# Optimization experiments

Hardware: AMD Instinct MI355X
Metric: run time of the kernel (lower is better)

Reference implementation:

```python
import jax, jax.numpy as jnp
import numpy as np
from jax import lax

WIN = 9  # NCC window per axis (default [9]*3)

# 3x3x3 edge/shape kernels, shape [O=1, I=1, 3, 3, 3]
_LAP = np.zeros((3, 3, 3), np.float32)
_LAP[1, 1, 1] = 6.0
_LAP[0, 1, 1] = _LAP[2, 1, 1] = -1.0
_LAP[1, 0, 1] = _LAP[1, 2, 1] = -1.0
_LAP[1, 1, 0] = _LAP[1, 1, 2] = -1.0
LAP_K = jnp.asarray(_LAP)[None, None]

_row = np.array([[-1.0, 0.0, 1.0], [-2.0, 0.0, 2.0], [-1.0, 0.0, 1.0]], np.float32)
SOBEL_X = jnp.asarray(np.stack([_row, _row, _row], axis=0))[None, None]
_plane = np.array([[-1.0, -2.0, -1.0], [-1.0, -2.0, -1.0], [-1.0, -2.0, -1.0]], np.float32)
SOBEL_Y = jnp.asarray(np.stack([_plane, np.zeros((3, 3), np.float32), -_plane], axis=0))[None, None]
_zp = np.array([[-1.0, -1.0, -1.0], [0.0, 0.0, 0.0], [1.0, 1.0, 1.0]], np.float32)
SOBEL_Z = jnp.asarray(np.stack([_zp, 2.0 * _zp, _zp], axis=0))[None, None]


def conv3d(x, k, pad):
    # x: [N,C,D,H,W], k: [O,I,kd,kh,kw]
    return lax.conv_general_dilated(x, k, (1, 1, 1), [(pad, pad)] * 3)


def box_sum(x, win=WIN):
    # Separable all-ones box filter == dense ones conv (same math, fewer FLOPs)
    pad = win // 2
    for axis in range(3):
        kshape = [1, 1, 1, 1, 1]
        kshape[2 + axis] = win
        k = jnp.ones(kshape, x.dtype)
        padding = [(pad, pad) if a == axis else (0, 0) for a in range(3)]
        x = lax.conv_general_dilated(x, k, (1, 1, 1), padding)
    return x


def ncc_vxm(Ii, Ji, win=WIN):
    win_size = float(win ** 3)
    I2, J2, IJ = Ii * Ii, Ji * Ji, Ii * Ji
    I_sum = box_sum(Ii, win)
    J_sum = box_sum(Ji, win)
    I2_sum = box_sum(I2, win)
    J2_sum = box_sum(J2, win)
    IJ_sum = box_sum(IJ, win)
    u_I = I_sum / win_size
    u_J = J_sum / win_size
    cross = IJ_sum - u_J * I_sum - u_I * J_sum + u_I * u_J * win_size
    I_var = I2_sum - 2.0 * u_I * I_sum + u_I * u_I * win_size
    J_var = J2_sum - 2.0 * u_J * J_sum + u_J * u_J * win_size
    cc = cross * cross / (I_var * J_var + 1e-5)
    return -jnp.mean(cc)


def edge_detection(v):
    return conv3d(v, LAP_K, pad=1)


def shape_detection(v):
    gx = conv3d(v, SOBEL_X, pad=1)
    gy = conv3d(v, SOBEL_Y, pad=1)
    gz = conv3d(v, SOBEL_Z, pad=1)
    return jnp.sqrt(gx * gx + gy * gy + gz * gz)


def setup_inputs() -> dict:
    key = jax.random.key(0)
    k1, k2 = jax.random.split(key)
    shape = (1, 1, 160, 192, 160)
    y_true = jax.random.uniform(k1, shape, dtype=jnp.float32)
    y_pred = jax.random.uniform(k2, shape, dtype=jnp.float32)
    return {"y_true": y_true, "y_pred": y_pred}


def reference(y_true, y_pred):
    loss_orig = ncc_vxm(y_true, y_pred)
    loss_edge = ncc_vxm(edge_detection(y_true), edge_detection(y_pred))
    loss_shape = ncc_vxm(shape_detection(y_true), shape_detection(y_pred))
    return 0.8 * loss_orig + 0.1 * loss_edge + 0.1 * loss_shape
```

## Files before the change

### kernel.cpp

```cpp
#include <hip/hip_runtime.h>
#include <hip/hip_fp16.h>
#include <math.h>

#define DD 160
#define HHH 192
#define WWW 160
constexpr int HW = HHH * WWW;
constexpr int NV = DD * HHH * WWW;
constexpr int W4 = WWW / 4;
constexpr int HC = 4;
constexpr int DC = 4;
constexpr int SC = 5;

constexpr int NB_WH  = (W4 * DD * (HHH / HC)) / 256;
constexpr int NB_SO  = (W4 * HHH * (DD / SC)) / 256;
constexpr int NB_LAP = (NV / 4) / 256;
constexpr int NB_DCC = (W4 * HHH * (DD / DC)) / 256;

__device__ __forceinline__ float4 ldg4(const float* __restrict__ p, int idx, bool ok) {
    float4 z = make_float4(0.f, 0.f, 0.f, 0.f);
    return ok ? *(const float4*)(p + idx) : z;
}

__device__ __forceinline__ void st_h4(__half* __restrict__ t, int idx,
                                      float s0, float s1, float s2, float s3) {
    union { __half2 h2[2]; uint2 u; } pk;
    pk.h2[0] = __floats2half2_rn(s0, s1);
    pk.h2[1] = __floats2half2_rn(s2, s3);
    *(uint2*)(t + idx) = pk.u;
}

__device__ __forceinline__ void ld_h4(const __half* __restrict__ t, int idx, float o[4]) {
    union { __half2 h2[2]; uint2 u; } pk;
    pk.u = *(const uint2*)(t + idx);
    o[0] = __low2float(pk.h2[0]); o[1] = __high2float(pk.h2[0]);
    o[2] = __low2float(pk.h2[1]); o[3] = __high2float(pk.h2[1]);
}

__device__ __forceinline__ void lap_body(int t, const float* __restrict__ a,
                                         const float* __restrict__ b,
                                         __half* __restrict__ oa, __half* __restrict__ ob) {
    int w = (t % W4) * 4;
    int h = (t / W4) % HHH;
    int d = t / (W4 * HHH);
    int idx = (d * HHH + h) * WWW + w;
    bool dok0 = d > 0, dok1 = d < DD - 1, hok0 = h > 0, hok1 = h < HHH - 1;
#pragma unroll
    for (int s = 0; s < 2; s++) {
        const float* p = s ? b : a;
        __half* o = s ? ob : oa;
        float4 c = *(const float4*)(p + idx);
        float m1 = (w > 0) ? p[idx - 1] : 0.f;
        float p4 = (w + 4 < WWW) ? p[idx + 4] : 0.f;
        float4 dm = ldg4(p, idx - HW, dok0);
        float4 dp = ldg4(p, idx + HW, dok1);
        float4 hm = ldg4(p, idx - WWW, hok0);
        float4 hp = ldg4(p, idx + WWW, hok1);
        st_h4(o, idx,
              6.f * c.x - (m1 + c.y + dm.x + dp.x + hm.x + hp.x),
              6.f * c.y - (c.x + c.z + dm.y + dp.y + hm.y + hp.y),
              6.f * c.z - (c.y + c.w + dm.z + dp.z + hm.z + hp.z),
              6.f * c.w - (c.z + p4 + dm.w + dp.w + hm.w + hp.w));
    }
}

__device__ __forceinline__ void sobel_slice(const float* __restrict__ p, int s, int h, int w,
                                            float a1[4], float a2[4], float a3[4]) {
#pragma unroll
    for (int k = 0; k < 4; k++) { a1[k] = 0.f; a2[k] = 0.f; a3[k] = 0.f; }
#pragma unroll
    for (int kh = -1; kh <= 1; kh++) {
        int h2 = h + kh;
        if ((unsigned)h2 < (unsigned)HHH) {
            int rb = (s * HHH + h2) * WWW + w;
            float4 cen = *(const float4*)(p + rb);
            float xm = (w > 0) ? p[rb - 1] : 0.f;
            float xp = (w + 4 < WWW) ? p[rb + 4] : 0.f;
            float xv[6] = {xm, cen.x, cen.y, cen.z, cen.w, xp};
            float smh = (kh == 0) ? 2.f : 1.f;
            float grh = (float)kh;
#pragma unroll
            for (int k = 0; k < 4; k++) {
                float gw = xv[k + 2] - xv[k];
                float pw = xv[k] + xv[k + 1] + xv[k + 2];
                float sw = pw + xv[k + 1];
                a1[k] += smh * gw;
                a2[k] += sw;
                a3[k] += grh * pw;
            }
        }
    }
}

__device__ __forceinline__ void sobel_body(int t, const float* __restrict__ a,
                                           const float* __restrict__ b,
                                           __half* __restrict__ oa, __half* __restrict__ ob) {
    int w = (t % W4) * 4;
    int h = (t / W4) % HHH;
    int c = t / (W4 * HHH);
    int d0 = c * SC;

    float A1[2][3][4], A2[2][3][4], A3[2][3][4];
#pragma unroll
    for (int r = 0; r < 2; r++)
#pragma unroll
        for (int j = 0; j < 3; j++)
#pragma unroll
            for (int k = 0; k < 4; k++) { A1[r][j][k] = 0.f; A2[r][j][k] = 0.f; A3[r][j][k] = 0.f; }

#pragma unroll
    for (int i = 0; i < SC + 2; i++) {
        int s = d0 - 1 + i;
#pragma unroll
        for (int r = 0; r < 2; r++)
#pragma unroll
            for (int k = 0; k < 4; k++) {
                A1[r][0][k] = A1[r][1][k]; A2[r][0][k] = A2[r][1][k]; A3[r][0][k] = A3[r][1][k];
                A1[r][1][k] = A1[r][2][k]; A2[r][1][k] = A2[r][2][k]; A3[r][1][k] = A3[r][2][k];
            }
        if (s >= 0 && s < DD) {
            sobel_slice(a, s, h, w, A1[0][2], A2[0][2], A3[0][2]);
            sobel_slice(b, s, h, w, A1[1][2], A2[1][2], A3[1][2]);
        } else {
#pragma unroll
            for (int r = 0; r < 2; r++)
#pragma unroll
                for (int k = 0; k < 4; k++) { A1[r][2][k] = 0.f; A2[r][2][k] = 0.f; A3[r][2][k] = 0.f; }
        }
        if (i >= 2) {
            int d = s - 1;
            int idx = (d * HHH + h) * WWW + w;
            float va[4], vb[4];
#pragma unroll
            for (int k = 0; k < 4; k++) {
                float gx = A1[0][0][k] + A1[0][1][k] + A1[0][2][k];
                float gy = A2[0][2][k] - A2[0][0][k];
                float gz = A3[0][0][k] + 2.f * A3[0][1][k] + A3[0][2][k];
                va[k] = sqrtf(gx * gx + gy * gy + gz * gz);
                gx = A1[1][0][k] + A1[1][1][k] + A1[1][2][k];
                gy = A2[1][2][k] - A2[1][0][k];
                gz = A3[1][0][k] + 2.f * A3[1][1][k] + A3[1][2][k];
                vb[k] = sqrtf(gx * gx + gy * gy + gz * gz);
            }
            st_h4(oa, idx, va[0], va[1], va[2], va[3]);
            st_h4(ob, idx, vb[0], vb[1], vb[2], vb[3]);
        }
    }
}

__device__ __forceinline__ void q5_from(const float x[12], const float y[12], float q[5][4]) {
    float s0 = 0, s1 = 0, s2 = 0, s3 = 0, s4 = 0;
#pragma unroll
    for (int j = 0; j < 9; j++) {
        s0 += x[j]; s1 += y[j];
        s2 += x[j] * x[j]; s3 += y[j] * y[j]; s4 += x[j] * y[j];
    }
    q[0][0] = s0; q[1][0] = s1; q[2][0] = s2; q[3][0] = s3; q[4][0] = s4;
#pragma unroll
    for (int k = 1; k < 4; k++) {
        q[0][k] = q[0][k - 1] + x[k + 8] - x[k - 1];
        q[1][k] = q[1][k - 1] + y[k + 8] - y[k - 1];
        q[2][k] = q[2][k - 1] + x[k + 8] * x[k + 8] - x[k - 1] * x[k - 1];
        q[3][k] = q[3][k - 1] + y[k + 8] * y[k + 8] - y[k - 1] * y[k - 1];
        q[4][k] = q[4][k - 1] + x[k + 8] * y[k + 8] - x[k - 1] * y[k - 1];
    }
}

__device__ __forceinline__ void ld12(const float* __restrict__ p, int rowbase, int w, float x[12]) {
    bool lo = (w >= 4);
    bool hi = (w + 7 < WWW);
    float4 x0 = ldg4(p, rowbase + w - 4, lo);
    float4 x1 = *(const float4*)(p + rowbase + w);
    float4 x2 = ldg4(p, rowbase + w + 4, hi);
    x[0] = x0.x; x[1] = x0.y; x[2] = x0.z; x[3] = x0.w;
    x[4] = x1.x; x[5] = x1.y; x[6] = x1.z; x[7] = x1.w;
    x[8] = x2.x; x[9] = x2.y; x[10] = x2.z; x[11] = x2.w;
}

__device__ __forceinline__ void ld12(const __half* __restrict__ p, int rowbase, int w, float x[12]) {
    bool lo = (w >= 4);
    bool hi = (w + 7 < WWW);
    union { __half2 h2[2]; uint2 u; } u0, u1, u2;
    uint2 z = make_uint2(0, 0);
    u0.u = lo ? *(const uint2*)(p + rowbase + w - 4) : z;
    u1.u = *(const uint2*)(p + rowbase + w);
    u2.u = hi ? *(const uint2*)(p + rowbase + w + 4) : z;
    x[0] = __low2float(u0.h2[0]); x[1] = __high2float(u0.h2[0]);
    x[2] = __low2float(u0.h2[1]); x[3] = __high2float(u0.h2[1]);
    x[4] = __low2float(u1.h2[0]); x[5] = __high2float(u1.h2[0]);
    x[6] = __low2float(u1.h2[1]); x[7] = __high2float(u1.h2[1]);
    x[8] = __low2float(u2.h2[0]); x[9] = __high2float(u2.h2[0]);
    x[10] = __low2float(u2.h2[1]); x[11] = __high2float(u2.h2[1]);
}

template <typename T>
__device__ __forceinline__ void rowq5(const T* __restrict__ a, const T* __restrict__ b,
                                      int rowbase, int w, float q[5][4]) {
    float x[12], y[12];
    ld12(a, rowbase, w, x);
    ld12(b, rowbase, w, y);
    q5_from(x, y, q);
}

template <typename T>
__device__ void whsum_body(int t, const T* __restrict__ a, const T* __restrict__ b,
                           __half* __restrict__ t0, __half* __restrict__ t1,
                           __half* __restrict__ t2, __half* __restrict__ t3,
                           __half* __restrict__ t4) {
    int w = (t % W4) * 4;
    int d = (t / W4) % DD;
    int c = t / (W4 * DD);
    int h0 = c * HC;

    float S[5][4] = {{0}};
    for (int j = 0; j < 9; j++) {
        int r = h0 - 4 + j;
        if ((unsigned)r < (unsigned)HHH) {
            float q[5][4];
            rowq5(a, b, (d * HHH + r) * WWW, w, q);
#pragma unroll
            for (int qq = 0; qq < 5; qq++)
#pragma unroll
                for (int k = 0; k < 4; k++) S[qq][k] += q[qq][k];
        }
    }
    {
        int idx = (d * HHH + h0) * WWW + w;
        st_h4(t0, idx, S[0][0], S[0][1], S[0][2], S[0][3]);
        st_h4(t1, idx, S[1][0], S[1][1], S[1][2], S[1][3]);
        st_h4(t2, idx, S[2][0], S[2][1], S[2][2], S[2][3]);
        st_h4(t3, idx, S[3][0], S[3][1], S[3][2], S[3][3]);
        st_h4(t4, idx, S[4][0], S[4][1], S[4][2], S[4][3]);
    }
    for (int h = h0 + 1; h < h0 + HC; h++) {
        int rin = h + 4, rout = h - 5;
        if (rin < HHH) {
            float q[5][4];
            rowq5(a, b, (d * HHH + rin) * WWW, w, q);
#pragma unroll
            for (int qq = 0; qq < 5; qq++)
#pragma unroll
                for (int k = 0; k < 4; k++) S[qq][k] += q[qq][k];
        }
        if (rout >= 0) {
            float q[5][4];
            rowq5(a, b, (d * HHH + rout) * WWW, w, q);
#pragma unroll
            for (int qq = 0; qq < 5; qq++)
#pragma unroll
                for (int k = 0; k < 4; k++) S[qq][k] -= q[qq][k];
        }
        int idx = (d * HHH + h) * WWW + w;
        st_h4(t0, idx, S[0][0], S[0][1], S[0][2], S[0][3]);
        st_h4(t1, idx, S[1][0], S[1][1], S[1][2], S[1][3]);
        st_h4(t2, idx, S[2][0], S[2][1], S[2][2], S[2][3]);
        st_h4(t3, idx, S[3][0], S[3][1], S[3][2], S[3][3]);
        st_h4(t4, idx, S[4][0], S[4][1], S[4][2], S[4][3]);
    }
}

__device__ __forceinline__ float cc1(float s0, float s1, float s2, float s3, float s4) {
    const float wsz = 729.0f;
    const float inv = 1.0f / 729.0f;
    float uI = s0 * inv;
    float uJ = s1 * inv;
    float cross = s4 - uJ * s0 - uI * s1 + uI * uJ * wsz;
    float Iv = s2 - 2.0f * uI * s0 + uI * uI * wsz;
    float Jv = s3 - 2.0f * uJ * s1 + uJ * uJ * wsz;
    return cross * cross / (Iv * Jv + 1e-5f);
}

__device__ void dcc_body(int t, const __half* __restrict__ t0, const __half* __restrict__ t1,
                         const __half* __restrict__ t2, const __half* __restrict__ t3,
                         const __half* __restrict__ t4, double* __restrict__ acc, int pair) {
    int w = (t % W4) * 4;
    int h = (t / W4) % HHH;
    int c = t / (W4 * HHH);
    int d0 = c * DC;

    float S[5][4] = {{0}};
    for (int j = 0; j < 9; j++) {
        int r = d0 - 4 + j;
        if ((unsigned)r < (unsigned)DD) {
            int idx = (r * HHH + h) * WWW + w;
            float v[5][4];
            ld_h4(t0, idx, v[0]); ld_h4(t1, idx, v[1]); ld_h4(t2, idx, v[2]);
            ld_h4(t3, idx, v[3]); ld_h4(t4, idx, v[4]);
#pragma unroll
            for (int q = 0; q < 5; q++)
#pragma unroll
                for (int k = 0; k < 4; k++) S[q][k] += v[q][k];
        }
    }
    float local = 0.f;
#pragma unroll
    for (int k = 0; k < 4; k++) local += cc1(S[0][k], S[1][k], S[2][k], S[3][k], S[4][k]);
#pragma unroll
    for (int d = 1; d < DC; d++) {
        int rin = d0 + d + 4, rout = d0 + d - 5;
        if (rin < DD) {
            int idx = (rin * HHH + h) * WWW + w;
            float v[5][4];
            ld_h4(t0, idx, v[0]); ld_h4(t1, idx, v[1]); ld_h4(t2, idx, v[2]);
            ld_h4(t3, idx, v[3]); ld_h4(t4, idx, v[4]);
#pragma unroll
            for (int q = 0; q < 5; q++)
#pragma unroll
                for (int k = 0; k < 4; k++) S[q][k] += v[q][k];
        }
        if (rout >= 0) {
            int idx = (rout * HHH + h) * WWW + w;
            float v[5][4];
            ld_h4(t0, idx, v[0]); ld_h4(t1, idx, v[1]); ld_h4(t2, idx, v[2]);
            ld_h4(t3, idx, v[3]); ld_h4(t4, idx, v[4]);
#pragma unroll
            for (int q = 0; q < 5; q++)
#pragma unroll
                for (int k = 0; k < 4; k++) S[q][k] -= v[q][k];
        }
#pragma unroll
        for (int k = 0; k < 4; k++) local += cc1(S[0][k], S[1][k], S[2][k], S[3][k], S[4][k]);
    }

    for (int off = 32; off > 0; off >>= 1) local += __shfl_down(local, off);
    __shared__ float wsum_[4];
    if ((threadIdx.x & 63) == 0) wsum_[threadIdx.x >> 6] = local;
    __syncthreads();
    if (threadIdx.x == 0) {
        float s = wsum_[0] + wsum_[1] + wsum_[2] + wsum_[3];
        atomicAdd(&acc[pair], (double)s);
    }
}

__global__ void stage1(const float* __restrict__ yt, const float* __restrict__ yp,
                       __half* __restrict__ e1a, __half* __restrict__ e1b,
                       __half* __restrict__ e2a, __half* __restrict__ e2b,
                       __half* __restrict__ ta0, __half* __restrict__ ta1,
                       __half* __restrict__ ta2, __half* __restrict__ ta3,
                       __half* __restrict__ ta4, double* __restrict__ acc) {
    int b = blockIdx.x;
    if (b < NB_WH) {
        whsum_body<float>(b * 256 + threadIdx.x, yt, yp, ta0, ta1, ta2, ta3, ta4);
    } else if (b < NB_WH + NB_SO) {
        sobel_body((b - NB_WH) * 256 + threadIdx.x, yt, yp, e2a, e2b);
    } else if (b < NB_WH + NB_SO + NB_LAP) {
        lap_body((b - NB_WH - NB_SO) * 256 + threadIdx.x, yt, yp, e1a, e1b);
    } else {
        if (threadIdx.x < 3) acc[threadIdx.x] = 0.0;
    }
}

__global__ void stage23(const __half* __restrict__ ea, const __half* __restrict__ eb,
                        __half* __restrict__ o0, __half* __restrict__ o1,
                        __half* __restrict__ o2, __half* __restrict__ o3,
                        __half* __restrict__ o4,
                        const __half* __restrict__ i0, const __half* __restrict__ i1,
                        const __half* __restrict__ i2, const __half* __restrict__ i3,
                        const __half* __restrict__ i4, double* __restrict__ acc, int pair) {
    int b = blockIdx.x;
    if (b < NB_WH) {
        whsum_body<__half>(b * 256 + threadIdx.x, ea, eb, o0, o1, o2, o3, o4);
    } else {
        dcc_body((b - NB_WH) * 256 + threadIdx.x, i0, i1, i2, i3, i4, acc, pair);
    }
}

__global__ void dcc_k(const __half* __restrict__ t0, const __half* __restrict__ t1,
                      const __half* __restrict__ t2, const __half* __restrict__ t3,
                      const __half* __restrict__ t4, double* __restrict__ acc, int pair) {
    dcc_body(blockIdx.x * 256 + threadIdx.x, t0, t1, t2, t3, t4, acc, pair);
}

__global__ void stage2b(const __half* __restrict__ e1a, const __half* __restrict__ e1b,
                        const __half* __restrict__ e2a, const __half* __restrict__ e2b,
                        __half* __restrict__ tB, __half* __restrict__ tC,
                        const __half* __restrict__ tA, double* __restrict__ acc) {
    int b = blockIdx.x;
    size_t nv = (size_t)NV;
    if (b < NB_WH) {
        whsum_body<__half>(b * 256 + threadIdx.x, e1a, e1b,
                           tB, tB + nv, tB + 2 * nv, tB + 3 * nv, tB + 4 * nv);
    } else if (b < 2 * NB_WH) {
        whsum_body<__half>((b - NB_WH) * 256 + threadIdx.x, e2a, e2b,
                           tC, tC + nv, tC + 2 * nv, tC + 3 * nv, tC + 4 * nv);
    } else {
        dcc_body((b - 2 * NB_WH) * 256 + threadIdx.x,
                 tA, tA + nv, tA + 2 * nv, tA + 3 * nv, tA + 4 * nv, acc, 0);
    }
}

__global__ void stage3b(const __half* __restrict__ tB, const __half* __restrict__ tC,
                        double* __restrict__ acc) {
    int b = blockIdx.x;
    size_t nv = (size_t)NV;
    if (b < NB_DCC) {
        dcc_body(b * 256 + threadIdx.x,
                 tB, tB + nv, tB + 2 * nv, tB + 3 * nv, tB + 4 * nv, acc, 1);
    } else {
        dcc_body((b - NB_DCC) * 256 + threadIdx.x,
                 tC, tC + nv, tC + 2 * nv, tC + 3 * nv, tC + 4 * nv, acc, 2);
    }
}

__global__ void finalize_k(const double* __restrict__ acc, float* __restrict__ out) {
    if (threadIdx.x == 0) {
        double v = 0.8 * acc[0] + 0.1 * acc[1] + 0.1 * acc[2];
        out[0] = (float)(-v / (double)NV);
    }
}

extern "C" void kernel_launch(void* const* d_in, const int* in_sizes, int n_in,
                              void* d_out, int out_size, void* d_ws, size_t ws_size,
                              hipStream_t stream) {
    const float* yt = (const float*)d_in[0];
    const float* yp = (const float*)d_in[1];
    float* out = (float*)d_out;

    double* acc = (double*)d_ws;
    __half* base = (__half*)((char*)d_ws + 256);
    size_t nv = (size_t)NV;
    __half* e1a = base + 0 * nv;
    __half* e1b = base + 1 * nv;
    __half* e2a = base + 2 * nv;
    __half* e2b = base + 3 * nv;
    __half* tA = base + 4 * nv;
    __half* tB = base + 9 * nv;
    __half* tC = base + 14 * nv;

    bool wide = ws_size >= 256 + 19 * nv * sizeof(__half);

    dim3 blk(256);

    hipLaunchKernelGGL(stage1, dim3(NB_WH + NB_SO + NB_LAP + 1), blk, 0, stream,
                       yt, yp, e1a, e1b, e2a, e2b,
                       tA, tA + nv, tA + 2 * nv, tA + 3 * nv, tA + 4 * nv, acc);

    if (wide) {
        hipLaunchKernelGGL(stage2b, dim3(2 * NB_WH + NB_DCC), blk, 0, stream,
                           e1a, e1b, e2a, e2b, tB, tC, tA, acc);
        hipLaunchKernelGGL(stage3b, dim3(2 * NB_DCC), blk, 0, stream, tB, tC, acc);
    } else {
        hipLaunchKernelGGL(stage23, dim3(NB_WH + NB_DCC), blk, 0, stream,
                           e1a, e1b,
                           tB, tB + nv, tB + 2 * nv, tB + 3 * nv, tB + 4 * nv,
                           tA, tA + nv, tA + 2 * nv, tA + 3 * nv, tA + 4 * nv,
                           acc, 0);
        hipLaunchKernelGGL(stage23, dim3(NB_WH + NB_DCC), blk, 0, stream,
                           e2a, e2b,
                           tA, tA + nv, tA + 2 * nv, tA + 3 * nv, tA + 4 * nv,
                           tB, tB + nv, tB + 2 * nv, tB + 3 * nv, tB + 4 * nv,
                           acc, 1);
        hipLaunchKernelGGL(dcc_k, dim3(NB_DCC), blk, 0, stream,
                           tA, tA + nv, tA + 2 * nv, tA + 3 * nv, tA + 4 * nv, acc, 2);
    }

    hipLaunchKernelGGL(finalize_k, dim3(1), dim3(1), 0, stream, acc, out);
}
```

Before: 375.2 us.

## Stage W/H box-sum input rows in LDS per (d, h-chunk) block

The W/H box-sum pass now assigns one block per depth slice and 24-row H chunk. Each block cooperatively loads the 32 needed rows of both inputs into shared memory, then 240 threads compute the sliding sums from LDS instead of re-reading overlapping rows and halo columns from global memory. This removes redundant global loads, at the cost of about 40KB of LDS per block, a barrier, 16 idle threads per block, and clamped scalar LDS reads in the inner loop.

New measurement: 675.2 us. 1.8x slower.

```diff
diff --git a/kernel.cpp b/kernel.cpp
--- a/kernel.cpp
+++ b/kernel.cpp
@@ -8,11 +8,12 @@
 constexpr int HW = HHH * WWW;
 constexpr int NV = DD * HHH * WWW;
 constexpr int W4 = WWW / 4;
-constexpr int HC = 4;
+constexpr int HCL = 24;
+constexpr int NROW = HCL + 8;
 constexpr int DC = 4;
 constexpr int SC = 5;
 
-constexpr int NB_WH  = (W4 * DD * (HHH / HC)) / 256;
+constexpr int NB_WH  = DD * (HHH / HCL);
 constexpr int NB_SO  = (W4 * HHH * (DD / SC)) / 256;
 constexpr int NB_LAP = (NV / 4) / 256;
 constexpr int NB_DCC = (W4 * HHH * (DD / DC)) / 256;
@@ -35,6 +36,16 @@
     pk.u = *(const uint2*)(t + idx);
     o[0] = __low2float(pk.h2[0]); o[1] = __high2float(pk.h2[0]);
     o[2] = __low2float(pk.h2[1]); o[3] = __high2float(pk.h2[1]);
+}
+
+__device__ __forceinline__ float4 ld4f(const float* __restrict__ p, int idx) {
+    return *(const float4*)(p + idx);
+}
+__device__ __forceinline__ float4 ld4f(const __half* __restrict__ p, int idx) {
+    union { __half2 h2[2]; uint2 u; } pk;
+    pk.u = *(const uint2*)(p + idx);
+    return make_float4(__low2float(pk.h2[0]), __high2float(pk.h2[0]),
+                       __low2float(pk.h2[1]), __high2float(pk.h2[1]));
 }
 
 __device__ __forceinline__ void lap_body(int t, const float* __restrict__ a,
@@ -166,96 +177,104 @@
     }
 }
 
-__device__ __forceinline__ void ld12(const float* __restrict__ p, int rowbase, int w, float x[12]) {
-    bool lo = (w >= 4);
-    bool hi = (w + 7 < WWW);
-    float4 x0 = ldg4(p, rowbase + w - 4, lo);
-    float4 x1 = *(const float4*)(p + rowbase + w);
-    float4 x2 = ldg4(p, rowbase + w + 4, hi);
-    x[0] = x0.x; x[1] = x0.y; x[2] = x0.z; x[3] = x0.w;
-    x[4] = x1.x; x[5] = x1.y; x[6] = x1.z; x[7] = x1.w;
-    x[8] = x2.x; x[9] = x2.y; x[10] = x2.z; x[11] = x2.w;
-}
-
-__device__ __forceinline__ void ld12(const __half* __restrict__ p, int rowbase, int w, float x[12]) {
-    bool lo = (w >= 4);
-    bool hi = (w + 7 < WWW);
-    union { __half2 h2[2]; uint2 u; } u0, u1, u2;
-    uint2 z = make_uint2(0, 0);
-    u0.u = lo ? *(const uint2*)(p + rowbase + w - 4) : z;
-    u1.u = *(const uint2*)(p + rowbase + w);
-    u2.u = hi ? *(const uint2*)(p + rowbase + w + 4) : z;
-    x[0] = __low2float(u0.h2[0]); x[1] = __high2float(u0.h2[0]);
-    x[2] = __low2float(u0.h2[1]); x[3] = __high2float(u0.h2[1]);
-    x[4] = __low2float(u1.h2[0]); x[5] = __high2float(u1.h2[0]);
-    x[6] = __low2float(u1.h2[1]); x[7] = __high2float(u1.h2[1]);
-    x[8] = __low2float(u2.h2[0]); x[9] = __high2float(u2.h2[0]);
-    x[10] = __low2float(u2.h2[1]); x[11] = __high2float(u2.h2[1]);
+__device__ __forceinline__ void ld12_lds(const float* __restrict__ row, int w, float x[12]) {
+#pragma unroll
+    for (int j = 0; j < 12; j++) {
+        int wi = w - 4 + j;
+        int wc = wi < 0 ? 0 : (wi > WWW - 1 ? WWW - 1 : wi);
+        float v = row[wc];
+        x[j] = ((unsigned)wi < (unsigned)WWW) ? v : 0.f;
+    }
 }
 
 template <typename T>
-__device__ __forceinline__ void rowq5(const T* __restrict__ a, const T* __restrict__ b,
-                                      int rowbase, int w, float q[5][4]) {
-    float x[12], y[12];
-    ld12(a, rowbase, w, x);
-    ld12(b, rowbase, w, y);
-    q5_from(x, y, q);
-}
-
-template <typename T>
-__device__ void whsum_body(int t, const T* __restrict__ a, const T* __restrict__ b,
-                           __half* __restrict__ t0, __half* __restrict__ t1,
-                           __half* __restrict__ t2, __half* __restrict__ t3,
-                           __half* __restrict__ t4) {
-    int w = (t % W4) * 4;
-    int d = (t / W4) % DD;
-    int c = t / (W4 * DD);
-    int h0 = c * HC;
-
-    float S[5][4] = {{0}};
-    for (int j = 0; j < 9; j++) {
-        int r = h0 - 4 + j;
+__device__ void whsum_lds_body(int blk, int tid, const T* __restrict__ a,
+                               const T* __restrict__ b,
+                               __half* __restrict__ t0, __half* __restrict__ t1,
+                               __half* __restrict__ t2, __half* __restrict__ t3,
+                               __half* __restrict__ t4) {
+    __shared__ float lds[2 * NROW * WWW];
+    int c = blk % (HHH / HCL);
+    int d = blk / (HHH / HCL);
+    int h0 = c * HCL;
+
+#pragma unroll
+    for (int k = 0; k < 10; k++) {
+        int i = tid + k * 256;
+        int arr = i / (NROW * W4);
+        int rem = i % (NROW * W4);
+        int row = rem / W4;
+        int f4i = rem % W4;
+        int r = h0 - 4 + row;
+        float4 v = make_float4(0.f, 0.f, 0.f, 0.f);
         if ((unsigned)r < (unsigned)HHH) {
-            float q[5][4];
-            rowq5(a, b, (d * HHH + r) * WWW, w, q);
+            int gidx = (d * HHH + r) * WWW + f4i * 4;
+            v = arr ? ld4f(b, gidx) : ld4f(a, gidx);
+        }
+        *(float4*)(&lds[(arr * NROW + row) * WWW + f4i * 4]) = v;
+    }
+    __syncthreads();
+
+    if (tid < 240) {
+        int w4 = tid % W4;
+        int s = tid / W4;
+        int w = w4 * 4;
+        int rbase = s * 4;
+        const float* lx = lds;
+        const float* ly = lds + NROW * WWW;
+
+        float S[5][4] = {{0}};
+        for (int j = 0; j < 9; j++) {
+            const float* rx = lx + (rbase + j) * WWW;
+            const float* ry = ly + (rbase + j) * WWW;
+            float x[12], y[12], q[5][4];
+            ld12_lds(rx, w, x);
+            ld12_lds(ry, w, y);
+            q5_from(x, y, q);
 #pragma unroll
             for (int qq = 0; qq < 5; qq++)
 #pragma unroll
                 for (int k = 0; k < 4; k++) S[qq][k] += q[qq][k];
         }
-    }
-    {
-        int idx = (d * HHH + h0) * WWW + w;
-        st_h4(t0, idx, S[0][0], S[0][1], S[0][2], S[0][3]);
-        st_h4(t1, idx, S[1][0], S[1][1], S[1][2], S[1][3]);
-        st_h4(t2, idx, S[2][0], S[2][1], S[2][2], S[2][3]);
-        st_h4(t3, idx, S[3][0], S[3][1], S[3][2], S[3][3]);
-        st_h4(t4, idx, S[4][0], S[4][1], S[4][2], S[4][3]);
-    }
-    for (int h = h0 + 1; h < h0 + HC; h++) {
-        int rin = h + 4, rout = h - 5;
-        if (rin < HHH) {
-            float q[5][4];
-            rowq5(a, b, (d * HHH + rin) * WWW, w, q);
-#pragma unroll
-            for (int qq = 0; qq < 5; qq++)
-#pragma unroll
-                for (int k = 0; k < 4; k++) S[qq][k] += q[qq][k];
-        }
-        if (rout >= 0) {
-            float q[5][4];
-            rowq5(a, b, (d * HHH + rout) * WWW, w, q);
-#pragma unroll
-            for (int qq = 0; qq < 5; qq++)
-#pragma unroll
-                for (int k = 0; k < 4; k++) S[qq][k] -= q[qq][k];
-        }
+        int h = h0 + s * 4;
         int idx = (d * HHH + h) * WWW + w;
         st_h4(t0, idx, S[0][0], S[0][1], S[0][2], S[0][3]);
         st_h4(t1, idx, S[1][0], S[1][1], S[1][2], S[1][3]);
         st_h4(t2, idx, S[2][0], S[2][1], S[2][2], S[2][3]);
         st_h4(t3, idx, S[3][0], S[3][1], S[3][2], S[3][3]);
         st_h4(t4, idx, S[4][0], S[4][1], S[4][2], S[4][3]);
+        for (int t = 1; t < 4; t++) {
+            {
+                const float* rx = lx + (rbase + 8 + t) * WWW;
+                const float* ry = ly + (rbase + 8 + t) * WWW;
+                float x[12], y[12], q[5][4];
+                ld12_lds(rx, w, x);
+                ld12_lds(ry, w, y);
+                q5_from(x, y, q);
+#pragma unroll
+                for (int qq = 0; qq < 5; qq++)
+#pragma unroll
+                    for (int k = 0; k < 4; k++) S[qq][k] += q[qq][k];
+            }
+            {
+                const float* rx = lx + (rbase + t - 1) * WWW;
+                const float* ry = ly + (rbase + t - 1) * WWW;
+                float x[12], y[12], q[5][4];
+                ld12_lds(rx, w, x);
+                ld12_lds(ry, w, y);
+                q5_from(x, y, q);
+#pragma unroll
+                for (int qq = 0; qq < 5; qq++)
+#pragma unroll
+                    for (int k = 0; k < 4; k++) S[qq][k] -= q[qq][k];
+            }
+            idx = (d * HHH + h + t) * WWW + w;
+            st_h4(t0, idx, S[0][0], S[0][1], S[0][2], S[0][3]);
+            st_h4(t1, idx, S[1][0], S[1][1], S[1][2], S[1][3]);
+            st_h4(t2, idx, S[2][0], S[2][1], S[2][2], S[2][3]);
+            st_h4(t3, idx, S[3][0], S[3][1], S[3][2], S[3][3]);
+            st_h4(t4, idx, S[4][0], S[4][1], S[4][2], S[4][3]);
+        }
     }
 }
 
@@ -340,7 +359,7 @@
                        __half* __restrict__ ta4, double* __restrict__ acc) {
     int b = blockIdx.x;
     if (b < NB_WH) {
-        whsum_body<float>(b * 256 + threadIdx.x, yt, yp, ta0, ta1, ta2, ta3, ta4);
+        whsum_lds_body<float>(b, threadIdx.x, yt, yp, ta0, ta1, ta2, ta3, ta4);
     } else if (b < NB_WH + NB_SO) {
         sobel_body((b - NB_WH) * 256 + threadIdx.x, yt, yp, e2a, e2b);
     } else if (b < NB_WH + NB_SO + NB_LAP) {
@@ -359,7 +378,7 @@
                         const __half* __restrict__ i4, double* __restrict__ acc, int pair) {
     int b = blockIdx.x;
     if (b < NB_WH) {
-        whsum_body<__half>(b * 256 + threadIdx.x, ea, eb, o0, o1, o2, o3, o4);
+        whsum_lds_body<__half>(b, threadIdx.x, ea, eb, o0, o1, o2, o3, o4);
     } else {
         dcc_body((b - NB_WH) * 256 + threadIdx.x, i0, i1, i2, i3, i4, acc, pair);
     }
@@ -378,11 +397,11 @@
     int b = blockIdx.x;
     size_t nv = (size_t)NV;
     if (b < NB_WH) {
-        whsum_body<__half>(b * 256 + threadIdx.x, e1a, e1b,
-                           tB, tB + nv, tB + 2 * nv, tB + 3 * nv, tB + 4 * nv);
+        whsum_lds_body<__half>(b, threadIdx.x, e1a, e1b,
+                               tB, tB + nv, tB + 2 * nv, tB + 3 * nv, tB + 4 * nv);
     } else if (b < 2 * NB_WH) {
-        whsum_body<__half>((b - NB_WH) * 256 + threadIdx.x, e2a, e2b,
-                           tC, tC + nv, tC + 2 * nv, tC + 3 * nv, tC + 4 * nv);
+        whsum_lds_body<__half>(b - NB_WH, threadIdx.x, e2a, e2b,
+                               tC, tC + nv, tC + 2 * nv, tC + 3 * nv, tC + 4 * nv);
     } else {
         dcc_body((b - 2 * NB_WH) * 256 + threadIdx.x,
                  tA, tA + nv, tA + 2 * nv, tA + 3 * nv, tA + 4 * nv, acc, 0);
```
